# Performance work log

Hardware: AMD Instinct MI355X
Metric: run time of the kernel (lower is better)

## Reference

```python
import jax, jax.numpy as jnp
import numpy as np

BATCH = 4096
IN_SIZES = [1024, 1024, 1024, 1024]
EMB = 2048  # embracement_size


def setup_inputs() -> dict:
    key = jax.random.key(0)
    keys = jax.random.split(key, 3 * len(IN_SIZES))
    inp = {}
    for i, d in enumerate(IN_SIZES):
        inp[f"x{i}"] = jax.random.normal(keys[3 * i], (BATCH, d), dtype=jnp.float32)
        # Linear params (Kaiming-ish scale)
        inp[f"W{i}"] = jax.random.normal(keys[3 * i + 1], (d, EMB), dtype=jnp.float32) / np.sqrt(d)
        inp[f"b{i}"] = jax.random.normal(keys[3 * i + 2], (EMB,), dtype=jnp.float32) * 0.01
    return inp


def _sample_indices(batch, num_feats, emb):
    # availabilities=None, selection_probabilities=None -> uniform p over modalities
    # multinomial(p, num_samples=emb, replacement=True) == categorical over log p
    logits = jnp.zeros((batch, num_feats), dtype=jnp.float32)  # uniform
    k = jax.random.key(42)
    # shape (emb, batch) broadcasts against logits batch shape (batch,)
    idx = jax.random.categorical(k, logits, axis=-1, shape=(emb, batch))
    return idx.T  # [batch, emb]


def reference(x0, W0, b0, x1, W1, b1, x2, W2, b2, x3, W3, b3):
    xs = [x0, x1, x2, x3]
    Ws = [W0, W1, W2, W3]
    bs = [b0, b1, b2, b3]
    # docking: Linear + ReLU per modality -> [batch, EMB, num_feats]
    dock = jnp.stack([jax.nn.relu(x @ W + b) for x, W, b in zip(xs, Ws, bs)], axis=-1)
    B, E, F = dock.shape
    idx = _sample_indices(B, F, E)  # [B, E] int32
    # gather along modality axis (replaces one-hot multiply-sum)
    out = jnp.take_along_axis(dock, idx[:, :, None], axis=-1)[..., 0]
    return out  # [batch, EMB]
```

## Files before the change

### kernel.cpp

```cpp
#include <hip/hip_runtime.h>
#include <stdint.h>


typedef short short8 __attribute__((ext_vector_type(8)));
typedef float floatx4 __attribute__((ext_vector_type(4)));

#define B_DIM 4096
#define K_DIM 1024
#define E_DIM 2048

__device__ __forceinline__ uint32_t rotl32(uint32_t x, uint32_t r) {
  return __builtin_amdgcn_alignbit(x, x, 32u - r);
}

__device__ __forceinline__ uint16_t f2bf(float x) {
  uint32_t u = __float_as_uint(x);
  u += 0x7FFFu + ((u >> 16) & 1u);
  return (uint16_t)(u >> 16);
}

__device__ __forceinline__ void threefry(uint32_t x0, uint32_t x1,
                                         uint32_t& o0, uint32_t& o1) {
  const uint32_t ks0 = 0u;
  const uint32_t ks1 = 42u;
  const uint32_t ks2 = 0x1BD11BDAu ^ 42u;
  x0 += ks0; x1 += ks1;
#define TF_R(r) { x0 += x1; x1 = rotl32(x1, r); x1 ^= x0; }
  TF_R(13) TF_R(15) TF_R(26) TF_R(6)
  x0 += ks1; x1 += ks2 + 1u;
  TF_R(17) TF_R(29) TF_R(16) TF_R(24)
  x0 += ks2; x1 += ks0 + 2u;
  TF_R(13) TF_R(15) TF_R(26) TF_R(6)
  x0 += ks0; x1 += ks1 + 3u;
  TF_R(17) TF_R(29) TF_R(16) TF_R(24)
  x0 += ks1; x1 += ks2 + 4u;
  TF_R(13) TF_R(15) TF_R(26) TF_R(6)
  x0 += ks2; x1 += ks0 + 5u;
#undef TF_R
  o0 = x0; o1 = x1;
}

__global__ __launch_bounds__(256) void prep_kernel(
    const float* __restrict__ x0, const float* __restrict__ x1,
    const float* __restrict__ x2, const float* __restrict__ x3,
    const float* __restrict__ W0, const float* __restrict__ W1,
    const float* __restrict__ W2, const float* __restrict__ W3,
    uint16_t* __restrict__ xb, uint16_t* __restrict__ Wt,
    uint8_t* __restrict__ idx1) {
  __shared__ float tile[32][33];
  const uint32_t g = blockIdx.x;
  const int t = threadIdx.x;
  const int f = g >> 11;
  const uint32_t ip = g & 2047u;

  const float* x = (f == 0) ? x0 : (f == 1) ? x1 : (f == 2) ? x2 : x3;
  const size_t xoff = ((size_t)ip * 256 + t) * 8;
  float4 v0 = *(const float4*)(x + xoff);
  float4 v1 = *(const float4*)(x + xoff + 4);

  const float* W = (f == 0) ? W0 : (f == 1) ? W1 : (f == 2) ? W2 : W3;
  const int e0 = (int)(ip & 63) * 32, k0 = (int)(ip >> 6) * 32;
  const int tx = t & 31, ty = t >> 5;
  float wv[4];
#pragma unroll
  for (int i = 0; i < 4; ++i)
    wv[i] = W[(size_t)(k0 + ty + i * 8) * E_DIM + e0 + tx];

  const uint32_t o0i = (g * 256u + t) * 4u;
  uint32_t byte = 0;
#pragma unroll
  for (uint32_t q = 0; q < 4; ++q) {
    uint32_t c = (o0i + q) << 2;
    uint32_t best = 0, bi = 0;
#pragma unroll
    for (uint32_t ff = 0; ff < 4; ++ff) {
      uint32_t y0, y1;
      threefry(0u, c + ff, y0, y1);
      uint32_t m = (y0 ^ y1) >> 9;
      if (ff == 0) best = m;
      else if (m > best) { best = m; bi = ff; }
    }
    byte |= bi << (2 * q);
  }
  idx1[g * 256u + t] = (uint8_t)byte;

  {
    union { uint16_t h[8]; uint64_t q[2]; } p;
    p.h[0] = f2bf(v0.x); p.h[1] = f2bf(v0.y);
    p.h[2] = f2bf(v0.z); p.h[3] = f2bf(v0.w);
    p.h[4] = f2bf(v1.x); p.h[5] = f2bf(v1.y);
    p.h[6] = f2bf(v1.z); p.h[7] = f2bf(v1.w);
    uint64_t* dst = (uint64_t*)(xb + (size_t)f * B_DIM * K_DIM + xoff);
    dst[0] = p.q[0]; dst[1] = p.q[1];
  }

#pragma unroll
  for (int i = 0; i < 4; ++i) tile[ty + i * 8][tx] = wv[i];
  __syncthreads();
  {
    const int el = t >> 3, kc = (t & 7) * 4;
    union { uint16_t h[4]; uint64_t q; } p;
#pragma unroll
    for (int i = 0; i < 4; ++i) p.h[i] = f2bf(tile[kc + i][el]);
    uint16_t* dst = Wt + (size_t)f * E_DIM * K_DIM;
    *(uint64_t*)(dst + (size_t)(e0 + el) * K_DIM + k0 + kc) = p.q;
  }
}

__device__ __forceinline__ void async16(const uint16_t* g, uint16_t* lds) {
  __builtin_amdgcn_global_load_lds(
      (const __attribute__((address_space(1))) void*)g,
      (__attribute__((address_space(3))) void*)lds, 16, 0, 0);
}

__global__ __launch_bounds__(256, 2) void gemm_fused(
    const uint16_t* __restrict__ Ab, const uint16_t* __restrict__ Bbt,
    const uint32_t* __restrict__ idx2,
    const float* __restrict__ bias0, const float* __restrict__ bias1,
    const float* __restrict__ bias2, const float* __restrict__ bias3,
    float* __restrict__ out) {
  __shared__ uint16_t As[2][128 * 64];
  __shared__ uint16_t Bs[2][128 * 64];

  const int tid = threadIdx.x;
  const int w = tid >> 6;
  const int l = tid & 63;

  const int flat = (int)(blockIdx.y * gridDim.x + blockIdx.x);
  const int swz = (flat & 7) * 64 + (flat >> 3);
  const int mBase = (swz >> 4) * 128;
  const int nBase = (swz & 15) * 128;

  const int wm = (w >> 1) * 64, wn = (w & 1) * 64;
  const int sr = l >> 3;
  const int skc = ((l & 7) ^ sr) * 8;
  const int fr = l & 15, fq = l >> 4;

  const int b_hi0 = (mBase + wm) >> 4;
  uint32_t iw[4][4];
#pragma unroll
  for (int ni = 0; ni < 4; ++ni) {
    int col = nBase + wn + ni * 16 + fr;
#pragma unroll
    for (int mi = 0; mi < 4; ++mi)
      iw[ni][mi] = idx2[(size_t)col * (B_DIM / 16) + b_hi0 + mi];
  }

  floatx4 res[4][4] = {};

#pragma unroll 1
  for (int f = 0; f < 4; ++f) {
    const uint16_t* A = Ab  + (size_t)f * B_DIM * K_DIM + (size_t)mBase * K_DIM;
    const uint16_t* B = Bbt + (size_t)f * E_DIM * K_DIM + (size_t)nBase * K_DIM;
    const uint16_t* Aw = A + (size_t)(32 * w + sr) * K_DIM + skc;
    const uint16_t* Bw = B + (size_t)(32 * w + sr) * K_DIM + skc;

    floatx4 acc[4][4] = {};

#pragma unroll
    for (int tt = 0; tt < 4; ++tt) {
      async16(Aw + (size_t)(8 * tt) * K_DIM, &As[0][(4 * w + tt) * 512]);
      async16(Bw + (size_t)(8 * tt) * K_DIM, &Bs[0][(4 * w + tt) * 512]);
    }
    __syncthreads();

    int buf = 0;
#pragma unroll 1
    for (int kt = 0; kt < 16; ++kt) {
      int kn = (kt + 1) * 64;
      if (kt + 1 < 16) {
#pragma unroll
        for (int tt = 0; tt < 4; ++tt) {
          async16(Aw + (size_t)(8 * tt) * K_DIM + kn, &As[buf ^ 1][(4 * w + tt) * 512]);
          async16(Bw + (size_t)(8 * tt) * K_DIM + kn, &Bs[buf ^ 1][(4 * w + tt) * 512]);
        }
      }
#pragma unroll
      for (int h = 0; h < 2; ++h) {
        short8 a[4], b[4];
        const int ch = h * 4 + fq;
#pragma unroll
        for (int mi = 0; mi < 4; ++mi) {
          int row = wm + mi * 16 + fr;
          a[mi] = *(const short8*)&As[buf][row * 64 + (ch ^ (fr & 7)) * 8];
        }
#pragma unroll
        for (int ni = 0; ni < 4; ++ni) {
          int row = wn + ni * 16 + fr;
          b[ni] = *(const short8*)&Bs[buf][row * 64 + (ch ^ (fr & 7)) * 8];
        }
#pragma unroll
        for (int mi = 0; mi < 4; ++mi)
#pragma unroll
          for (int ni = 0; ni < 4; ++ni)
            acc[mi][ni] = __builtin_amdgcn_mfma_f32_16x16x32_bf16(
                a[mi], b[ni], acc[mi][ni], 0, 0, 0);
      }
      __syncthreads();
      buf ^= 1;
    }

    const float* bias = (f == 0) ? bias0 : (f == 1) ? bias1
                      : (f == 2) ? bias2 : bias3;
#pragma unroll
    for (int ni = 0; ni < 4; ++ni) {
      float bvf = bias[nBase + wn + ni * 16 + fr];
#pragma unroll
      for (int mi = 0; mi < 4; ++mi) {
        uint32_t wd = iw[ni][mi];
#pragma unroll
        for (int r = 0; r < 4; ++r) {
          uint32_t sel = (wd >> (2 * (fq * 4 + r))) & 3u;
          if (sel == (uint32_t)f) res[mi][ni][r] = acc[mi][ni][r] + bvf;
        }
      }
    }
  }

#pragma unroll
  for (int ni = 0; ni < 4; ++ni) {
    int col = nBase + wn + ni * 16 + fr;
#pragma unroll
    for (int mi = 0; mi < 4; ++mi) {
      int row0 = mBase + wm + mi * 16 + fq * 4;
#pragma unroll
      for (int r = 0; r < 4; ++r) {
        float o = res[mi][ni][r];
        __builtin_nontemporal_store(o > 0.f ? o : 0.f,
                                    &out[(size_t)(row0 + r) * E_DIM + col]);
      }
    }
  }
}

extern "C" void kernel_launch(void* const* d_in, const int* in_sizes, int n_in,
                              void* d_out, int out_size, void* d_ws, size_t ws_size,
                              hipStream_t stream) {
  const float* x[4]; const float* W[4]; const float* bs[4];
  for (int f = 0; f < 4; ++f) {
    x[f]  = (const float*)d_in[3 * f + 0];
    W[f]  = (const float*)d_in[3 * f + 1];
    bs[f] = (const float*)d_in[3 * f + 2];
  }
  char* ws = (char*)d_ws;
  uint16_t* xb  = (uint16_t*)ws;
  uint16_t* Wt  = (uint16_t*)(ws + (size_t)32 * 1024 * 1024);
  uint8_t*  idx1 = (uint8_t*)(ws + (size_t)48 * 1024 * 1024);
  float* out = (float*)d_out;

  prep_kernel<<<dim3(8192), dim3(256), 0, stream>>>(
      x[0], x[1], x[2], x[3], W[0], W[1], W[2], W[3], xb, Wt, idx1);
  gemm_fused<<<dim3(E_DIM / 128, B_DIM / 128), dim3(256), 0, stream>>>(
      xb, Wt, (const uint32_t*)idx1, bs[0], bs[1], bs[2], bs[3], out);
}
```

Before: 254.2 us.

## Flatten modality/K loops into one pipelined stream with BK=32 and higher occupancy

```diff
diff --git a/kernel.cpp b/kernel.cpp
--- a/kernel.cpp
+++ b/kernel.cpp
@@ -113,14 +113,18 @@
       (__attribute__((address_space(3))) void*)lds, 16, 0, 0);
 }
 
-__global__ __launch_bounds__(256, 2) void gemm_fused(
+#define PLANE_A ((size_t)B_DIM * K_DIM)
+#define PLANE_B ((size_t)E_DIM * K_DIM)
+#define BK 32
+
+__global__ __launch_bounds__(256, 4) void gemm_fused(
     const uint16_t* __restrict__ Ab, const uint16_t* __restrict__ Bbt,
     const uint32_t* __restrict__ idx2,
     const float* __restrict__ bias0, const float* __restrict__ bias1,
     const float* __restrict__ bias2, const float* __restrict__ bias3,
     float* __restrict__ out) {
-  __shared__ uint16_t As[2][128 * 64];
-  __shared__ uint16_t Bs[2][128 * 64];
+  __shared__ uint16_t As[2][128 * BK];
+  __shared__ uint16_t Bs[2][128 * BK];
 
   const int tid = threadIdx.x;
   const int w = tid >> 6;
@@ -132,9 +136,24 @@
   const int nBase = (swz & 15) * 128;
 
   const int wm = (w >> 1) * 64, wn = (w & 1) * 64;
-  const int sr = l >> 3;
-  const int skc = ((l & 7) ^ sr) * 8;
   const int fr = l & 15, fq = l >> 4;
+
+  const int sRow = l >> 2;
+  const int gck = ((l & 3) ^ ((sRow >> 1) & 3)) * 8;
+  const uint16_t* aBase = Ab + (size_t)(mBase + 32 * w + sRow) * K_DIM + gck;
+  const uint16_t* bBase = Bbt + (size_t)(nBase + 32 * w + sRow) * K_DIM + gck;
+
+  const int kread = (fq ^ ((fr >> 1) & 3)) * 8;
+
+  auto stage = [&](int t, int bf) {
+    const int f = t >> 5, ko = (t & 31) * BK;
+    const uint16_t* pA = aBase + (size_t)f * PLANE_A + ko;
+    const uint16_t* pB = bBase + (size_t)f * PLANE_B + ko;
+    async16(pA, &As[bf][(2 * w + 0) * 512]);
+    async16(pA + (size_t)16 * K_DIM, &As[bf][(2 * w + 1) * 512]);
+    async16(pB, &Bs[bf][(2 * w + 0) * 512]);
+    async16(pB + (size_t)16 * K_DIM, &Bs[bf][(2 * w + 1) * 512]);
+  };
 
   const int b_hi0 = (mBase + wm) >> 4;
   uint32_t iw[4][4];
@@ -146,75 +165,53 @@
       iw[ni][mi] = idx2[(size_t)col * (B_DIM / 16) + b_hi0 + mi];
   }
 
+  floatx4 acc[4][4] = {};
   floatx4 res[4][4] = {};
 
+  stage(0, 0);
+  __syncthreads();
+
+  int buf = 0;
 #pragma unroll 1
-  for (int f = 0; f < 4; ++f) {
-    const uint16_t* A = Ab  + (size_t)f * B_DIM * K_DIM + (size_t)mBase * K_DIM;
-    const uint16_t* B = Bbt + (size_t)f * E_DIM * K_DIM + (size_t)nBase * K_DIM;
-    const uint16_t* Aw = A + (size_t)(32 * w + sr) * K_DIM + skc;
-    const uint16_t* Bw = B + (size_t)(32 * w + sr) * K_DIM + skc;
-
-    floatx4 acc[4][4] = {};
-
-#pragma unroll
-    for (int tt = 0; tt < 4; ++tt) {
-      async16(Aw + (size_t)(8 * tt) * K_DIM, &As[0][(4 * w + tt) * 512]);
-      async16(Bw + (size_t)(8 * tt) * K_DIM, &Bs[0][(4 * w + tt) * 512]);
-    }
-    __syncthreads();
-
-    int buf = 0;
-#pragma unroll 1
-    for (int kt = 0; kt < 16; ++kt) {
-      int kn = (kt + 1) * 64;
-      if (kt + 1 < 16) {
-#pragma unroll
-        for (int tt = 0; tt < 4; ++tt) {
-          async16(Aw + (size_t)(8 * tt) * K_DIM + kn, &As[buf ^ 1][(4 * w + tt) * 512]);
-          async16(Bw + (size_t)(8 * tt) * K_DIM + kn, &Bs[buf ^ 1][(4 * w + tt) * 512]);
-        }
-      }
-#pragma unroll
-      for (int h = 0; h < 2; ++h) {
-        short8 a[4], b[4];
-        const int ch = h * 4 + fq;
+  for (int j = 0; j < 128; ++j) {
+    if (j + 1 < 128) stage(j + 1, buf ^ 1);
+
+    short8 a[4], b[4];
+#pragma unroll
+    for (int mi = 0; mi < 4; ++mi)
+      a[mi] = *(const short8*)&As[buf][(wm + mi * 16 + fr) * BK + kread];
+#pragma unroll
+    for (int ni = 0; ni < 4; ++ni)
+      b[ni] = *(const short8*)&Bs[buf][(wn + ni * 16 + fr) * BK + kread];
+#pragma unroll
+    for (int mi = 0; mi < 4; ++mi)
+#pragma unroll
+      for (int ni = 0; ni < 4; ++ni)
+        acc[mi][ni] = __builtin_amdgcn_mfma_f32_16x16x32_bf16(
+            a[mi], b[ni], acc[mi][ni], 0, 0, 0);
+
+    if ((j & 31) == 31) {
+      const int f = j >> 5;
+      const float* bias = (f == 0) ? bias0 : (f == 1) ? bias1
+                        : (f == 2) ? bias2 : bias3;
+#pragma unroll
+      for (int ni = 0; ni < 4; ++ni) {
+        float bvf = bias[nBase + wn + ni * 16 + fr];
 #pragma unroll
         for (int mi = 0; mi < 4; ++mi) {
-          int row = wm + mi * 16 + fr;
-          a[mi] = *(const short8*)&As[buf][row * 64 + (ch ^ (fr & 7)) * 8];
-        }
-#pragma unroll
-        for (int ni = 0; ni < 4; ++ni) {
-          int row = wn + ni * 16 + fr;
-          b[ni] = *(const short8*)&Bs[buf][row * 64 + (ch ^ (fr & 7)) * 8];
-        }
-#pragma unroll
-        for (int mi = 0; mi < 4; ++mi)
-#pragma unroll
-          for (int ni = 0; ni < 4; ++ni)
-            acc[mi][ni] = __builtin_amdgcn_mfma_f32_16x16x32_bf16(
-                a[mi], b[ni], acc[mi][ni], 0, 0, 0);
-      }
-      __syncthreads();
-      buf ^= 1;
-    }
-
-    const float* bias = (f == 0) ? bias0 : (f == 1) ? bias1
-                      : (f == 2) ? bias2 : bias3;
-#pragma unroll
-    for (int ni = 0; ni < 4; ++ni) {
-      float bvf = bias[nBase + wn + ni * 16 + fr];
-#pragma unroll
-      for (int mi = 0; mi < 4; ++mi) {
-        uint32_t wd = iw[ni][mi];
-#pragma unroll
-        for (int r = 0; r < 4; ++r) {
-          uint32_t sel = (wd >> (2 * (fq * 4 + r))) & 3u;
-          if (sel == (uint32_t)f) res[mi][ni][r] = acc[mi][ni][r] + bvf;
+          uint32_t wd = iw[ni][mi];
+#pragma unroll
+          for (int r = 0; r < 4; ++r) {
+            uint32_t sel = (wd >> (2 * (fq * 4 + r))) & 3u;
+            if (sel == (uint32_t)f) res[mi][ni][r] = acc[mi][ni][r] + bvf;
+            acc[mi][ni][r] = 0.f;
+          }
         }
       }
     }
+
+    __syncthreads();
+    buf ^= 1;
   }
 
 #pragma unroll
```

Result: slower. 397.3 us (+56.3%).
